# Performance work log

Hardware: AMD Instinct MI355X
Metric: run time of the kernel (lower is better)

## Reference

```python
import jax, jax.numpy as jnp
import numpy as np

N = 50000   # nodes
E = 800000  # edges
D = 128     # input = hidden = output dim
G = 64      # graphs in batch


def setup_inputs() -> dict:
    key = jax.random.key(0)
    ks = jax.random.split(key, 12)
    s = 1.0 / np.sqrt(D)
    x = jax.random.normal(ks[0], (N, D), dtype=jnp.float32)
    edge_index = jax.random.randint(ks[1], (2, E), 0, N, dtype=jnp.int64)
    batch = jnp.sort(jax.random.randint(ks[2], (N,), 0, G, dtype=jnp.int64))
    return {
        "x": x,
        "W1": jax.random.normal(ks[3], (D, D), jnp.float32) * s,
        "b1": jnp.zeros((D,), jnp.float32),
        "W2": jax.random.normal(ks[4], (D, D), jnp.float32) * s,
        "b2": jnp.zeros((D,), jnp.float32),
        "W3": jax.random.normal(ks[5], (D, D), jnp.float32) * s,
        "b3": jnp.zeros((D,), jnp.float32),
        "Wm1": jax.random.normal(ks[6], (D, D), jnp.float32) * s,
        "bm1": jnp.zeros((D,), jnp.float32),
        "Wm2": jax.random.normal(ks[7], (D, D), jnp.float32) * s,
        "bm2": jnp.zeros((D,), jnp.float32),
        "edge_index": edge_index,
        "batch": batch,
    }


def _gcn_conv(x, W, b, src, dst, deg_isqrt, num_nodes):
    # PyG GCNConv: h = D^{-1/2}(A+I)D^{-1/2} X W + b  (self-loops included in src/dst)
    h = x @ W  # [N, Dout]
    norm = deg_isqrt[src] * deg_isqrt[dst]  # [E+N]
    msg = h[src] * norm[:, None]            # gather + scale
    out = jax.ops.segment_sum(msg, dst, num_segments=num_nodes)  # scatter-add
    return out + b


def reference(x, W1, b1, W2, b2, W3, b3, Wm1, bm1, Wm2, bm2, edge_index, batch):
    num_nodes = x.shape[0]
    loop = jnp.arange(num_nodes, dtype=edge_index.dtype)
    src = jnp.concatenate([edge_index[0], loop])  # add self-loops
    dst = jnp.concatenate([edge_index[1], loop])
    # degree with self-loops (edge_weight = 1), computed on target nodes
    deg = jax.ops.segment_sum(jnp.ones_like(dst, dtype=x.dtype), dst,
                              num_segments=num_nodes)
    deg_isqrt = jnp.where(deg > 0, jax.lax.rsqrt(deg), 0.0)

    h = jax.nn.relu(_gcn_conv(x, W1, b1, src, dst, deg_isqrt, num_nodes))
    h = jax.nn.relu(_gcn_conv(h, W2, b2, src, dst, deg_isqrt, num_nodes))
    h = _gcn_conv(h, W3, b3, src, dst, deg_isqrt, num_nodes)

    # global_mean_pool over graph ids
    sums = jax.ops.segment_sum(h, batch, num_segments=G)
    cnts = jax.ops.segment_sum(jnp.ones((num_nodes,), h.dtype), batch,
                               num_segments=G)
    pooled = sums / jnp.maximum(cnts, 1.0)[:, None]  # [G, D]

    out = jax.nn.relu(pooled @ Wm1 + bm1) @ Wm2 + bm2
    return out
```

## Files before the change

kernel.cpp:

```cpp
#include <hip/hip_runtime.h>
#include <hip/hip_bf16.h>

typedef __attribute__((ext_vector_type(8))) short short8;
typedef __attribute__((ext_vector_type(4))) float floatx4;

#define SLAB_CAP 96

static __device__ __forceinline__ ushort f2b(float f) {
    __hip_bfloat16 h = __float2bfloat16(f);
    return __builtin_bit_cast(ushort, h);
}
static __device__ __forceinline__ float blo(uint u) {
    return __builtin_bit_cast(float, u << 16);
}
static __device__ __forceinline__ float bhi(uint u) {
    return __builtin_bit_cast(float, u & 0xffff0000u);
}
static __device__ __forceinline__ uint pack2(float lo, float hi) {
    return (uint)f2b(lo) | ((uint)f2b(hi) << 16);
}

static __device__ __forceinline__ void fill_body(int bid, const int* __restrict__ src,
                                                 const int* __restrict__ dst, int E,
                                                 int* __restrict__ deg_cnt,
                                                 int* __restrict__ slab) {
    int e0 = (bid * 256 + threadIdx.x) * 4;
    if (e0 + 3 < E) {
        int4 s = *(const int4*)(src + e0);
        int4 d = *(const int4*)(dst + e0);
        int p0 = atomicAdd(&deg_cnt[d.x], 1);
        int p1 = atomicAdd(&deg_cnt[d.y], 1);
        int p2 = atomicAdd(&deg_cnt[d.z], 1);
        int p3 = atomicAdd(&deg_cnt[d.w], 1);
        if (p0 < SLAB_CAP) slab[d.x * SLAB_CAP + p0] = s.x;
        if (p1 < SLAB_CAP) slab[d.y * SLAB_CAP + p1] = s.y;
        if (p2 < SLAB_CAP) slab[d.z * SLAB_CAP + p2] = s.z;
        if (p3 < SLAB_CAP) slab[d.w * SLAB_CAP + p3] = s.w;
    } else {
        for (int e = e0; e < E; ++e) {
            int d = dst[e];
            int p = atomicAdd(&deg_cnt[d], 1);
            if (p < SLAB_CAP) slab[d * SLAB_CAP + p] = src[e];
        }
    }
}

template <typename XT, int SCALE>
static __device__ __forceinline__ void mm_body(ushort* __restrict__ wt,
                                               const XT* __restrict__ X,
                                               const float* __restrict__ W,
                                               const int* __restrict__ degp,
                                               ushort* __restrict__ Y,
                                               int N, int tiles, int tile0, int tstride) {
    int t = threadIdx.x;
    {
        int c0 = (t & 31) * 4;
        int k0 = (t >> 5) * 4;
#pragma unroll
        for (int i = 0; i < 4; i++) {
            int kk = k0 + i * 32;
            float4 r0 = *(const float4*)&W[(kk + 0) * 128 + c0];
            float4 r1 = *(const float4*)&W[(kk + 1) * 128 + c0];
            float4 r2 = *(const float4*)&W[(kk + 2) * 128 + c0];
            float4 r3 = *(const float4*)&W[(kk + 3) * 128 + c0];
            float colv[4][4] = {{r0.x, r1.x, r2.x, r3.x},
                                {r0.y, r1.y, r2.y, r3.y},
                                {r0.z, r1.z, r2.z, r3.z},
                                {r0.w, r1.w, r2.w, r3.w}};
#pragma unroll
            for (int j = 0; j < 4; j++) {
                int c = c0 + j;
                int chs = (kk >> 3) ^ (c & 7);
                int idx = c * 128 + (chs << 3) + (kk & 7);
                ushort4 v;
                v.x = f2b(colv[j][0]); v.y = f2b(colv[j][1]);
                v.z = f2b(colv[j][2]); v.w = f2b(colv[j][3]);
                *(ushort4*)&wt[idx] = v;
            }
        }
    }
    __syncthreads();
    int wv = t >> 6;
    int l  = t & 63;
    int lr = l & 15;
    int lk = l >> 4;
    for (int tile = tile0; tile < tiles; tile += tstride) {
        int row = tile * 64 + wv * 16 + lr;
        int rowc = row < N ? row : N - 1;
        short8 a[4];
#pragma unroll
        for (int ks = 0; ks < 4; ks++) {
            int kb = lk * 8 + ks * 32;
            if constexpr (sizeof(XT) == 4) {
                const float* p = (const float*)X + (size_t)rowc * 128 + kb;
                float4 f0 = *(const float4*)p;
                float4 f1 = *(const float4*)(p + 4);
                short8 av;
                av[0] = (short)f2b(f0.x); av[1] = (short)f2b(f0.y);
                av[2] = (short)f2b(f0.z); av[3] = (short)f2b(f0.w);
                av[4] = (short)f2b(f1.x); av[5] = (short)f2b(f1.y);
                av[6] = (short)f2b(f1.z); av[7] = (short)f2b(f1.w);
                a[ks] = av;
            } else {
                a[ks] = *(const short8*)((const ushort*)X + (size_t)rowc * 128 + kb);
            }
        }
        floatx4 acc[8];
#pragma unroll
        for (int ct = 0; ct < 8; ct++) acc[ct] = (floatx4)(0.f);
#pragma unroll
        for (int ct = 0; ct < 8; ct++) {
            int col = ct * 16 + lr;
#pragma unroll
            for (int ks = 0; ks < 4; ks++) {
                int kb = lk * 8 + ks * 32;
                int chs = (kb >> 3) ^ (col & 7);
                short8 b = *(const short8*)&wt[col * 128 + (chs << 3)];
                acc[ct] = __builtin_amdgcn_mfma_f32_16x16x32_bf16(a[ks], b, acc[ct], 0, 0, 0);
            }
        }
        int rbase = tile * 64 + wv * 16 + lk * 4;
        float dr[4] = {1.f, 1.f, 1.f, 1.f};
        if constexpr (SCALE) {
            if (rbase + 3 < N) {
                int4 d4 = *(const int4*)&degp[rbase];
                dr[0] = rsqrtf((float)(d4.x + 1)); dr[1] = rsqrtf((float)(d4.y + 1));
                dr[2] = rsqrtf((float)(d4.z + 1)); dr[3] = rsqrtf((float)(d4.w + 1));
            } else {
#pragma unroll
                for (int r = 0; r < 4; r++)
                    dr[r] = rbase + r < N ? rsqrtf((float)(degp[rbase + r] + 1)) : 0.f;
            }
        }
#pragma unroll
        for (int ct = 0; ct < 8; ct++) {
#pragma unroll
            for (int r = 0; r < 4; r++) {
                int ro = rbase + r;
                if (ro < N) Y[(size_t)ro * 128 + ct * 16 + lr] = f2b(acc[ct][r] * dr[r]);
            }
        }
    }
}

__global__ __launch_bounds__(256) void k_fill_mm(const int* __restrict__ src,
                                                 const int* __restrict__ dst, int E,
                                                 int* __restrict__ deg_cnt,
                                                 int* __restrict__ slab,
                                                 const float* __restrict__ X,
                                                 const float* __restrict__ W,
                                                 ushort* __restrict__ Y,
                                                 int N, int tiles, int fillBlocks) {
    __shared__ ushort wt[128 * 128];
    int bid = blockIdx.x;
    if (bid < fillBlocks) {
        fill_body(bid, src, dst, E, deg_cnt, slab);
        return;
    }
    mm_body<float, 0>(wt, X, W, nullptr, Y, N, tiles, bid - fillBlocks, gridDim.x - fillBlocks);
}

template <typename XT, int SCALE>
__global__ __launch_bounds__(256) void k_matmul_mfma(const XT* __restrict__ X,
                                                     const float* __restrict__ W,
                                                     const int* __restrict__ degp,
                                                     ushort* __restrict__ Y,
                                                     int N, int tiles) {
    __shared__ ushort wt[128 * 128];
    mm_body<XT, SCALE>(wt, X, W, degp, Y, N, tiles, blockIdx.x, gridDim.x);
}

template <int MODE>
__global__ __launch_bounds__(256) void k_aggregate(const uint* __restrict__ H,
                                                   const int* __restrict__ deg_cnt,
                                                   const int* __restrict__ slab,
                                                   const float* __restrict__ bias,
                                                   uint* __restrict__ Y,
                                                   const int* __restrict__ batch,
                                                   float* __restrict__ psums, int N) {
    int t = threadIdx.x;
    int node = blockIdx.x * 4 + (t >> 6);
    int lane = t & 63;
    bool valid = node < N;
    float ax = 0.f, ay = 0.f;
    if (valid) {
        int degn = deg_cnt[node];
        float din = rsqrtf((float)(degn + 1));
        uint hv = H[(size_t)node * 64 + lane];
        if constexpr (MODE == 0) { ax = din * blo(hv); ay = din * bhi(hv); }
        else { ax = blo(hv); ay = bhi(hv); }
        int deg = degn > SLAB_CAP ? SLAB_CAP : degn;
        const int* row = slab + (size_t)node * SLAB_CAP;
        int e = 0;
        if constexpr (MODE == 0) {
            for (; e + 3 < deg; e += 4) {
                int4 i0 = *(const int4*)(row + e);
                int d0 = deg_cnt[i0.x], d1 = deg_cnt[i0.y];
                int d2 = deg_cnt[i0.z], d3 = deg_cnt[i0.w];
                uint g0 = H[(size_t)i0.x * 64 + lane];
                uint g1 = H[(size_t)i0.y * 64 + lane];
                uint g2 = H[(size_t)i0.z * 64 + lane];
                uint g3 = H[(size_t)i0.w * 64 + lane];
                float w0 = rsqrtf((float)(d0 + 1)), w1 = rsqrtf((float)(d1 + 1));
                float w2 = rsqrtf((float)(d2 + 1)), w3 = rsqrtf((float)(d3 + 1));
                ax += blo(g0) * w0 + blo(g1) * w1 + blo(g2) * w2 + blo(g3) * w3;
                ay += bhi(g0) * w0 + bhi(g1) * w1 + bhi(g2) * w2 + bhi(g3) * w3;
            }
            for (; e < deg; ++e) {
                int s = row[e];
                float ws = rsqrtf((float)(deg_cnt[s] + 1));
                uint g = H[(size_t)s * 64 + lane];
                ax += blo(g) * ws; ay += bhi(g) * ws;
            }
        } else {
            float bx = 0.f, by = 0.f;
            for (; e + 7 < deg; e += 8) {
                int4 i0 = *(const int4*)(row + e);
                int4 i1 = *(const int4*)(row + e + 4);
                uint g0 = H[(size_t)i0.x * 64 + lane];
                uint g1 = H[(size_t)i0.y * 64 + lane];
                uint g2 = H[(size_t)i0.z * 64 + lane];
                uint g3 = H[(size_t)i0.w * 64 + lane];
                uint g4 = H[(size_t)i1.x * 64 + lane];
                uint g5 = H[(size_t)i1.y * 64 + lane];
                uint g6 = H[(size_t)i1.z * 64 + lane];
                uint g7 = H[(size_t)i1.w * 64 + lane];
                ax += blo(g0) + blo(g1) + blo(g2) + blo(g3);
                ay += bhi(g0) + bhi(g1) + bhi(g2) + bhi(g3);
                bx += blo(g4) + blo(g5) + blo(g6) + blo(g7);
                by += bhi(g4) + bhi(g5) + bhi(g6) + bhi(g7);
            }
            for (; e + 3 < deg; e += 4) {
                int4 i0 = *(const int4*)(row + e);
                uint g0 = H[(size_t)i0.x * 64 + lane];
                uint g1 = H[(size_t)i0.y * 64 + lane];
                uint g2 = H[(size_t)i0.z * 64 + lane];
                uint g3 = H[(size_t)i0.w * 64 + lane];
                ax += blo(g0) + blo(g1) + blo(g2) + blo(g3);
                ay += bhi(g0) + bhi(g1) + bhi(g2) + bhi(g3);
            }
            for (; e < deg; ++e) {
                uint g = H[(size_t)row[e] * 64 + lane];
                ax += blo(g); ay += bhi(g);
            }
            ax += bx; ay += by;
        }
        float2 b = *(const float2*)&bias[lane * 2];
        ax = ax * din + b.x; ay = ay * din + b.y;
        if constexpr (MODE != 2) {
            ax = fmaxf(ax, 0.f); ay = fmaxf(ay, 0.f);
            Y[(size_t)node * 64 + lane] = pack2(ax, ay);
        }
    }
    if constexpr (MODE == 2) {
        __shared__ float ls[128];
        if (t < 128) ls[t] = 0.f;
        __syncthreads();
        int nbase = blockIdx.x * 4;
        if (nbase >= N) return;
        int nlast = nbase + 3 < N ? nbase + 3 : N - 1;
        int gf = batch[nbase], gl = batch[nlast];
        if (gf == gl) {
            if (valid) {
                atomicAdd(&ls[lane * 2], ax);
                atomicAdd(&ls[lane * 2 + 1], ay);
            }
            __syncthreads();
            if (t < 128) atomicAdd(&psums[gf * 128 + t], ls[t]);
        } else {
            if (valid) {
                int g = batch[node];
                atomicAdd(&psums[g * 128 + lane * 2], ax);
                atomicAdd(&psums[g * 128 + lane * 2 + 1], ay);
            }
        }
    }
}

__global__ __launch_bounds__(128) void k_mlp(const float* __restrict__ sums,
                                             const int* __restrict__ batch, int N,
                                             const float* __restrict__ Wm1,
                                             const float* __restrict__ bm1,
                                             const float* __restrict__ Wm2,
                                             const float* __restrict__ bm2,
                                             float* __restrict__ out) {
    __shared__ float p[128], t1[128];
    int g = blockIdx.x, j = threadIdx.x;
    int n0, n1;
    {
        int lo = 0, hi = N;
        while (lo < hi) { int m = (lo + hi) >> 1; if (batch[m] < g) lo = m + 1; else hi = m; }
        n0 = lo;
        hi = N;
        while (lo < hi) { int m = (lo + hi) >> 1; if (batch[m] < g + 1) lo = m + 1; else hi = m; }
        n1 = lo;
    }
    float cnt = (float)(n1 - n0);
    p[j] = sums[g * 128 + j] / fmaxf(cnt, 1.0f);
    __syncthreads();
    float acc = bm1[j];
#pragma unroll 4
    for (int k = 0; k < 128; k++) acc += p[k] * Wm1[k * 128 + j];
    t1[j] = fmaxf(acc, 0.f);
    __syncthreads();
    float acc2 = bm2[j];
#pragma unroll 4
    for (int k = 0; k < 128; k++) acc2 += t1[k] * Wm2[k * 128 + j];
    out[g * 128 + j] = acc2;
}

extern "C" void kernel_launch(void* const* d_in, const int* in_sizes, int n_in,
                              void* d_out, int out_size, void* d_ws, size_t ws_size,
                              hipStream_t stream) {
    const float* x   = (const float*)d_in[0];
    const float* W1  = (const float*)d_in[1];
    const float* b1  = (const float*)d_in[2];
    const float* W2  = (const float*)d_in[3];
    const float* b2  = (const float*)d_in[4];
    const float* W3  = (const float*)d_in[5];
    const float* b3  = (const float*)d_in[6];
    const float* Wm1 = (const float*)d_in[7];
    const float* bm1 = (const float*)d_in[8];
    const float* Wm2 = (const float*)d_in[9];
    const float* bm2 = (const float*)d_in[10];
    const int* edge  = (const int*)d_in[11];
    const int* batch = (const int*)d_in[12];

    int N = in_sizes[0] / 128;
    int E = in_sizes[11] / 2;
    int G = out_size / 128;
    const int* esrc = edge;
    const int* edst = edge + E;

    char* w = (char*)d_ws;
    auto alloc = [&](size_t bytes) -> char* {
        char* p = w;
        w += (bytes + 255) & ~size_t(255);
        return p;
    };
    ushort* Hb     = (ushort*)alloc((size_t)N * 128 * 2);
    ushort* Gb     = (ushort*)alloc((size_t)N * 128 * 2);
    int*    slab   = (int*)alloc((size_t)N * SLAB_CAP * 4);
    char*  zbase   = w;
    int*   deg_cnt = (int*)alloc((size_t)N * 4);
    float* psums   = (float*)alloc((size_t)G * 128 * 4);
    size_t zbytes  = (size_t)(w - zbase);

    hipMemsetAsync(zbase, 0, zbytes, stream);

    int tiles64 = (N + 63) / 64;
    int fillBlocks = (E + 1023) / 1024;

    k_fill_mm<<<fillBlocks + tiles64, 256, 0, stream>>>(esrc, edst, E, deg_cnt, slab,
                                                        x, W1, Gb, N, tiles64, fillBlocks);
    k_aggregate<0><<<(N + 3) / 4, 256, 0, stream>>>((const uint*)Gb, deg_cnt, slab, b1,
                                                    (uint*)Hb, nullptr, nullptr, N);
    k_matmul_mfma<ushort, 1><<<tiles64, 256, 0, stream>>>(Hb, W2, deg_cnt, Gb, N, tiles64);
    k_aggregate<1><<<(N + 3) / 4, 256, 0, stream>>>((const uint*)Gb, deg_cnt, slab, b2,
                                                    (uint*)Hb, nullptr, nullptr, N);
    k_matmul_mfma<ushort, 1><<<tiles64, 256, 0, stream>>>(Hb, W3, deg_cnt, Gb, N, tiles64);
    k_aggregate<2><<<(N + 3) / 4, 256, 0, stream>>>((const uint*)Gb, deg_cnt, slab, b3,
                                                    nullptr, batch, psums, N);

    k_mlp<<<G, 128, 0, stream>>>(psums, batch, N, Wm1, bm1, Wm2, bm2, (float*)d_out);
}
```

Baseline: 324.9 us.

## Fuse whole GCN pipeline into one persistent cooperative kernel with grid syncs

Replaces the chain of separate launches (memset, fill+matmul, three aggregations, two matmuls, MLP) with a single cooperative persistent kernel that zeroes buffers itself and separates phases with grid.sync(). The first-layer aggregation is restructured: a separate prescale pass multiplies H by the source-node deg^-1/2 so all layers can use the unweighted aggregation path. A non-cooperative multi-kernel fallback is kept. The aim is to remove launch gaps and tail effects; the cost is that grid-wide barriers and a fixed, occupancy-limited grid size (launch bounds 256,4) may lower latency hiding in the gather-heavy aggregations and make the fill/matmul split less balanced.

```diff
diff --git a/kernel.cpp b/kernel.cpp
--- a/kernel.cpp
+++ b/kernel.cpp
@@ -1,5 +1,8 @@
 #include <hip/hip_runtime.h>
 #include <hip/hip_bf16.h>
+#include <hip/hip_cooperative_groups.h>
+
+namespace cg = cooperative_groups;
 
 typedef __attribute__((ext_vector_type(8))) short short8;
 typedef __attribute__((ext_vector_type(4))) float floatx4;
@@ -20,11 +23,11 @@
     return (uint)f2b(lo) | ((uint)f2b(hi) << 16);
 }
 
-static __device__ __forceinline__ void fill_body(int bid, const int* __restrict__ src,
-                                                 const int* __restrict__ dst, int E,
-                                                 int* __restrict__ deg_cnt,
-                                                 int* __restrict__ slab) {
-    int e0 = (bid * 256 + threadIdx.x) * 4;
+static __device__ __forceinline__ void fill_chunk(int c, const int* __restrict__ src,
+                                                  const int* __restrict__ dst, int E,
+                                                  int* __restrict__ deg_cnt,
+                                                  int* __restrict__ slab) {
+    int e0 = c * 1024 + threadIdx.x * 4;
     if (e0 + 3 < E) {
         int4 s = *(const int4*)(src + e0);
         int4 d = *(const int4*)(dst + e0);
@@ -143,77 +146,32 @@
     }
 }
 
-__global__ __launch_bounds__(256) void k_fill_mm(const int* __restrict__ src,
-                                                 const int* __restrict__ dst, int E,
-                                                 int* __restrict__ deg_cnt,
-                                                 int* __restrict__ slab,
-                                                 const float* __restrict__ X,
-                                                 const float* __restrict__ W,
-                                                 ushort* __restrict__ Y,
-                                                 int N, int tiles, int fillBlocks) {
-    __shared__ ushort wt[128 * 128];
-    int bid = blockIdx.x;
-    if (bid < fillBlocks) {
-        fill_body(bid, src, dst, E, deg_cnt, slab);
-        return;
-    }
-    mm_body<float, 0>(wt, X, W, nullptr, Y, N, tiles, bid - fillBlocks, gridDim.x - fillBlocks);
-}
-
-template <typename XT, int SCALE>
-__global__ __launch_bounds__(256) void k_matmul_mfma(const XT* __restrict__ X,
-                                                     const float* __restrict__ W,
-                                                     const int* __restrict__ degp,
-                                                     ushort* __restrict__ Y,
-                                                     int N, int tiles) {
-    __shared__ ushort wt[128 * 128];
-    mm_body<XT, SCALE>(wt, X, W, degp, Y, N, tiles, blockIdx.x, gridDim.x);
-}
-
 template <int MODE>
-__global__ __launch_bounds__(256) void k_aggregate(const uint* __restrict__ H,
-                                                   const int* __restrict__ deg_cnt,
-                                                   const int* __restrict__ slab,
-                                                   const float* __restrict__ bias,
-                                                   uint* __restrict__ Y,
-                                                   const int* __restrict__ batch,
-                                                   float* __restrict__ psums, int N) {
+static __device__ void agg_body(const uint* __restrict__ H,
+                                const int* __restrict__ deg_cnt,
+                                const int* __restrict__ slab,
+                                const float* __restrict__ bias,
+                                uint* __restrict__ Y,
+                                const int* __restrict__ batch,
+                                float* __restrict__ psums,
+                                int N, int bid, int nb) {
+    __shared__ float ls[128];
     int t = threadIdx.x;
-    int node = blockIdx.x * 4 + (t >> 6);
     int lane = t & 63;
-    bool valid = node < N;
-    float ax = 0.f, ay = 0.f;
-    if (valid) {
-        int degn = deg_cnt[node];
-        float din = rsqrtf((float)(degn + 1));
-        uint hv = H[(size_t)node * 64 + lane];
-        if constexpr (MODE == 0) { ax = din * blo(hv); ay = din * bhi(hv); }
-        else { ax = blo(hv); ay = bhi(hv); }
-        int deg = degn > SLAB_CAP ? SLAB_CAP : degn;
-        const int* row = slab + (size_t)node * SLAB_CAP;
-        int e = 0;
-        if constexpr (MODE == 0) {
-            for (; e + 3 < deg; e += 4) {
-                int4 i0 = *(const int4*)(row + e);
-                int d0 = deg_cnt[i0.x], d1 = deg_cnt[i0.y];
-                int d2 = deg_cnt[i0.z], d3 = deg_cnt[i0.w];
-                uint g0 = H[(size_t)i0.x * 64 + lane];
-                uint g1 = H[(size_t)i0.y * 64 + lane];
-                uint g2 = H[(size_t)i0.z * 64 + lane];
-                uint g3 = H[(size_t)i0.w * 64 + lane];
-                float w0 = rsqrtf((float)(d0 + 1)), w1 = rsqrtf((float)(d1 + 1));
-                float w2 = rsqrtf((float)(d2 + 1)), w3 = rsqrtf((float)(d3 + 1));
-                ax += blo(g0) * w0 + blo(g1) * w1 + blo(g2) * w2 + blo(g3) * w3;
-                ay += bhi(g0) * w0 + bhi(g1) * w1 + bhi(g2) * w2 + bhi(g3) * w3;
-            }
-            for (; e < deg; ++e) {
-                int s = row[e];
-                float ws = rsqrtf((float)(deg_cnt[s] + 1));
-                uint g = H[(size_t)s * 64 + lane];
-                ax += blo(g) * ws; ay += bhi(g) * ws;
-            }
-        } else {
+    int groups = (N + 3) >> 2;
+    for (int ga = bid; ga < groups; ga += nb) {
+        int node = ga * 4 + (t >> 6);
+        bool valid = node < N;
+        float ax = 0.f, ay = 0.f;
+        if (valid) {
+            int degn = deg_cnt[node];
+            float din = rsqrtf((float)(degn + 1));
+            uint hv = H[(size_t)node * 64 + lane];
+            ax = blo(hv); ay = bhi(hv);
             float bx = 0.f, by = 0.f;
+            int deg = degn > SLAB_CAP ? SLAB_CAP : degn;
+            const int* row = slab + (size_t)node * SLAB_CAP;
+            int e = 0;
             for (; e + 7 < deg; e += 8) {
                 int4 i0 = *(const int4*)(row + e);
                 int4 i1 = *(const int4*)(row + e + 4);
@@ -244,69 +202,201 @@
                 ax += blo(g); ay += bhi(g);
             }
             ax += bx; ay += by;
-        }
-        float2 b = *(const float2*)&bias[lane * 2];
-        ax = ax * din + b.x; ay = ay * din + b.y;
-        if constexpr (MODE != 2) {
-            ax = fmaxf(ax, 0.f); ay = fmaxf(ay, 0.f);
-            Y[(size_t)node * 64 + lane] = pack2(ax, ay);
-        }
-    }
-    if constexpr (MODE == 2) {
-        __shared__ float ls[128];
-        if (t < 128) ls[t] = 0.f;
+            float2 b = *(const float2*)&bias[lane * 2];
+            ax = ax * din + b.x; ay = ay * din + b.y;
+            if constexpr (MODE == 1) {
+                ax = fmaxf(ax, 0.f); ay = fmaxf(ay, 0.f);
+                Y[(size_t)node * 64 + lane] = pack2(ax, ay);
+            }
+        }
+        if constexpr (MODE == 2) {
+            if (t < 128) ls[t] = 0.f;
+            __syncthreads();
+            int nbase = ga * 4;
+            if (nbase < N) {
+                int nlast = nbase + 3 < N ? nbase + 3 : N - 1;
+                int gf = batch[nbase], gl = batch[nlast];
+                if (gf == gl) {
+                    if (valid) {
+                        atomicAdd(&ls[lane * 2], ax);
+                        atomicAdd(&ls[lane * 2 + 1], ay);
+                    }
+                    __syncthreads();
+                    if (t < 128) atomicAdd(&psums[gf * 128 + t], ls[t]);
+                    __syncthreads();
+                } else {
+                    if (valid) {
+                        int g = batch[node];
+                        atomicAdd(&psums[g * 128 + lane * 2], ax);
+                        atomicAdd(&psums[g * 128 + lane * 2 + 1], ay);
+                    }
+                    __syncthreads();
+                }
+            }
+        }
+    }
+}
+
+static __device__ void mlp_body(const float* __restrict__ sums,
+                                const int* __restrict__ batch, int N, int G,
+                                const float* __restrict__ Wm1, const float* __restrict__ bm1,
+                                const float* __restrict__ Wm2, const float* __restrict__ bm2,
+                                float* __restrict__ out, int bid, int nb) {
+    __shared__ float p[128], t1[128];
+    int t = threadIdx.x;
+    for (int g = bid; g < G; g += nb) {
+        int n0, n1;
+        {
+            int lo = 0, hi = N;
+            while (lo < hi) { int m = (lo + hi) >> 1; if (batch[m] < g) lo = m + 1; else hi = m; }
+            n0 = lo;
+            hi = N;
+            while (lo < hi) { int m = (lo + hi) >> 1; if (batch[m] < g + 1) lo = m + 1; else hi = m; }
+            n1 = lo;
+        }
+        if (t < 128) {
+            float cnt = (float)(n1 - n0);
+            p[t] = sums[g * 128 + t] / fmaxf(cnt, 1.0f);
+        }
         __syncthreads();
-        int nbase = blockIdx.x * 4;
-        if (nbase >= N) return;
-        int nlast = nbase + 3 < N ? nbase + 3 : N - 1;
-        int gf = batch[nbase], gl = batch[nlast];
-        if (gf == gl) {
-            if (valid) {
-                atomicAdd(&ls[lane * 2], ax);
-                atomicAdd(&ls[lane * 2 + 1], ay);
-            }
-            __syncthreads();
-            if (t < 128) atomicAdd(&psums[gf * 128 + t], ls[t]);
+        if (t < 128) {
+            float acc = bm1[t];
+#pragma unroll 4
+            for (int k = 0; k < 128; k++) acc += p[k] * Wm1[k * 128 + t];
+            t1[t] = fmaxf(acc, 0.f);
+        }
+        __syncthreads();
+        if (t < 128) {
+            float acc2 = bm2[t];
+#pragma unroll 4
+            for (int k = 0; k < 128; k++) acc2 += t1[k] * Wm2[k * 128 + t];
+            out[g * 128 + t] = acc2;
+        }
+        __syncthreads();
+    }
+}
+
+__global__ __launch_bounds__(256, 4) void k_gnn(
+    const float* __restrict__ x,
+    const float* __restrict__ W1, const float* __restrict__ b1,
+    const float* __restrict__ W2, const float* __restrict__ b2,
+    const float* __restrict__ W3, const float* __restrict__ b3,
+    const float* __restrict__ Wm1, const float* __restrict__ bm1,
+    const float* __restrict__ Wm2, const float* __restrict__ bm2,
+    const int* __restrict__ esrc, const int* __restrict__ edst,
+    const int* __restrict__ batch,
+    int N, int E, int G,
+    int* __restrict__ deg_cnt, int* __restrict__ slab,
+    ushort* __restrict__ Hb, ushort* __restrict__ Gb,
+    float* __restrict__ psums, float* __restrict__ out) {
+    cg::grid_group grid = cg::this_grid();
+    __shared__ ushort wt[128 * 128];
+    int bid = blockIdx.x, nb = gridDim.x, t = threadIdx.x;
+    int tiles = (N + 63) >> 6;
+
+    {
+        int ztot = N + G * 128;
+        for (int i = bid * 256 + t; i < ztot; i += nb * 256) {
+            if (i < N) deg_cnt[i] = 0; else psums[i - N] = 0.f;
+        }
+    }
+    grid.sync();
+
+    {
+        int F = nb >> 1;
+        int C = (E + 1023) >> 10;
+        if (bid < F) {
+            for (int c = bid; c < C; c += F) fill_chunk(c, esrc, edst, E, deg_cnt, slab);
         } else {
-            if (valid) {
-                int g = batch[node];
-                atomicAdd(&psums[g * 128 + lane * 2], ax);
-                atomicAdd(&psums[g * 128 + lane * 2 + 1], ay);
-            }
-        }
-    }
-}
-
-__global__ __launch_bounds__(128) void k_mlp(const float* __restrict__ sums,
-                                             const int* __restrict__ batch, int N,
-                                             const float* __restrict__ Wm1,
-                                             const float* __restrict__ bm1,
-                                             const float* __restrict__ Wm2,
-                                             const float* __restrict__ bm2,
-                                             float* __restrict__ out) {
-    __shared__ float p[128], t1[128];
-    int g = blockIdx.x, j = threadIdx.x;
-    int n0, n1;
+            mm_body<float, 0>(wt, x, W1, nullptr, Gb, N, tiles, bid - F, nb - F);
+        }
+    }
+    grid.sync();
+
     {
-        int lo = 0, hi = N;
-        while (lo < hi) { int m = (lo + hi) >> 1; if (batch[m] < g) lo = m + 1; else hi = m; }
-        n0 = lo;
-        hi = N;
-        while (lo < hi) { int m = (lo + hi) >> 1; if (batch[m] < g + 1) lo = m + 1; else hi = m; }
-        n1 = lo;
-    }
-    float cnt = (float)(n1 - n0);
-    p[j] = sums[g * 128 + j] / fmaxf(cnt, 1.0f);
-    __syncthreads();
-    float acc = bm1[j];
-#pragma unroll 4
-    for (int k = 0; k < 128; k++) acc += p[k] * Wm1[k * 128 + j];
-    t1[j] = fmaxf(acc, 0.f);
-    __syncthreads();
-    float acc2 = bm2[j];
-#pragma unroll 4
-    for (int k = 0; k < 128; k++) acc2 += t1[k] * Wm2[k * 128 + j];
-    out[g * 128 + j] = acc2;
+        const uint* s = (const uint*)Gb;
+        uint* d = (uint*)Hb;
+        int tot = N * 64;
+        for (int i = bid * 256 + t; i < tot; i += nb * 256) {
+            int n = i >> 6;
+            float din = rsqrtf((float)(deg_cnt[n] + 1));
+            uint u = s[i];
+            d[i] = pack2(blo(u) * din, bhi(u) * din);
+        }
+    }
+    grid.sync();
+
+    agg_body<1>((const uint*)Hb, deg_cnt, slab, b1, (uint*)Gb, nullptr, nullptr, N, bid, nb);
+    grid.sync();
+
+    mm_body<ushort, 1>(wt, Gb, W2, deg_cnt, Hb, N, tiles, bid, nb);
+    grid.sync();
+
+    agg_body<1>((const uint*)Hb, deg_cnt, slab, b2, (uint*)Gb, nullptr, nullptr, N, bid, nb);
+    grid.sync();
+
+    mm_body<ushort, 1>(wt, Gb, W3, deg_cnt, Hb, N, tiles, bid, nb);
+    grid.sync();
+
+    agg_body<2>((const uint*)Hb, deg_cnt, slab, b3, nullptr, batch, psums, N, bid, nb);
+    grid.sync();
+
+    mlp_body(psums, batch, N, G, Wm1, bm1, Wm2, bm2, out, bid, nb);
+}
+
+__global__ __launch_bounds__(256) void k_fillmm_s(const int* __restrict__ src,
+                                                  const int* __restrict__ dst, int E,
+                                                  int* __restrict__ deg_cnt,
+                                                  int* __restrict__ slab,
+                                                  const float* __restrict__ X,
+                                                  const float* __restrict__ W,
+                                                  ushort* __restrict__ Y,
+                                                  int N, int tiles, int fillBlocks) {
+    __shared__ ushort wt[128 * 128];
+    int bid = blockIdx.x;
+    if (bid < fillBlocks) { fill_chunk(bid, src, dst, E, deg_cnt, slab); return; }
+    mm_body<float, 0>(wt, X, W, nullptr, Y, N, tiles, bid - fillBlocks, gridDim.x - fillBlocks);
+}
+
+__global__ __launch_bounds__(256) void k_prescale_s(const int* __restrict__ deg_cnt,
+                                                    const uint* __restrict__ s,
+                                                    uint* __restrict__ d, int N) {
+    int i = blockIdx.x * 256 + threadIdx.x;
+    if (i >= N * 64) return;
+    int n = i >> 6;
+    float din = rsqrtf((float)(deg_cnt[n] + 1));
+    uint u = s[i];
+    d[i] = pack2(blo(u) * din, bhi(u) * din);
+}
+
+template <typename XT, int SCALE>
+__global__ __launch_bounds__(256) void k_mm_s(const XT* __restrict__ X,
+                                              const float* __restrict__ W,
+                                              const int* __restrict__ degp,
+                                              ushort* __restrict__ Y, int N, int tiles) {
+    __shared__ ushort wt[128 * 128];
+    mm_body<XT, SCALE>(wt, X, W, degp, Y, N, tiles, blockIdx.x, gridDim.x);
+}
+
+template <int MODE>
+__global__ __launch_bounds__(256) void k_agg_s(const uint* __restrict__ H,
+                                               const int* __restrict__ deg_cnt,
+                                               const int* __restrict__ slab,
+                                               const float* __restrict__ bias,
+                                               uint* __restrict__ Y,
+                                               const int* __restrict__ batch,
+                                               float* __restrict__ psums, int N) {
+    agg_body<MODE>(H, deg_cnt, slab, bias, Y, batch, psums, N, blockIdx.x, gridDim.x);
+}
+
+__global__ __launch_bounds__(256) void k_mlp_s(const float* __restrict__ sums,
+                                               const int* __restrict__ batch, int N, int G,
+                                               const float* __restrict__ Wm1,
+                                               const float* __restrict__ bm1,
+                                               const float* __restrict__ Wm2,
+                                               const float* __restrict__ bm2,
+                                               float* __restrict__ out) {
+    mlp_body(sums, batch, N, G, Wm1, bm1, Wm2, bm2, out, blockIdx.x, gridDim.x);
 }
 
 extern "C" void kernel_launch(void* const* d_in, const int* in_sizes, int n_in,
@@ -331,6 +421,7 @@
     int G = out_size / 128;
     const int* esrc = edge;
     const int* edst = edge + E;
+    float* out = (float*)d_out;
 
     char* w = (char*)d_ws;
     auto alloc = [&](size_t bytes) -> char* {
@@ -346,21 +437,46 @@
     float* psums   = (float*)alloc((size_t)G * 128 * 4);
     size_t zbytes  = (size_t)(w - zbase);
 
+    int tiles = (N + 63) / 64;
+    int C = (E + 1023) / 1024;
+
+    int perCU = 0, cus = 0, dev = 0;
+    hipGetDevice(&dev);
+    hipDeviceGetAttribute(&cus, hipDeviceAttributeMultiprocessorCount, dev);
+    hipError_t qerr = hipOccupancyMaxActiveBlocksPerMultiprocessor(&perCU, k_gnn, 256, 0);
+    bool coop_ok = (qerr == hipSuccess) && perCU >= 1 && cus >= 1;
+    if (coop_ok) {
+        int nb = perCU * cus;
+        if (nb > 2048) nb = 2048;
+        if (nb < 8) coop_ok = false;
+        if (coop_ok) {
+            const float *a0 = x, *a1 = W1, *a2 = b1, *a3 = W2, *a4 = b2, *a5 = W3, *a6 = b3;
+            const float *a7 = Wm1, *a8 = bm1, *a9 = Wm2, *a10 = bm2;
+            const int *a11 = esrc, *a12 = edst, *a13 = batch;
+            int a14 = N, a15 = E, a16 = G;
+            int *a17 = deg_cnt, *a18 = slab;
+            ushort *a19 = Hb, *a20 = Gb;
+            float *a21 = psums, *a22 = out;
+            void* args[] = {&a0, &a1, &a2, &a3, &a4, &a5, &a6, &a7, &a8, &a9, &a10,
+                            &a11, &a12, &a13, &a14, &a15, &a16, &a17, &a18, &a19,
+                            &a20, &a21, &a22};
+            hipError_t lerr = hipLaunchCooperativeKernel((const void*)k_gnn, dim3(nb),
+                                                         dim3(256), args, 0, stream);
+            if (lerr == hipSuccess) return;
+        }
+    }
+
     hipMemsetAsync(zbase, 0, zbytes, stream);
-
-    int tiles64 = (N + 63) / 64;
-    int fillBlocks = (E + 1023) / 1024;
-
-    k_fill_mm<<<fillBlocks + tiles64, 256, 0, stream>>>(esrc, edst, E, deg_cnt, slab,
-                                                        x, W1, Gb, N, tiles64, fillBlocks);
-    k_aggregate<0><<<(N + 3) / 4, 256, 0, stream>>>((const uint*)Gb, deg_cnt, slab, b1,
-                                                    (uint*)Hb, nullptr, nullptr, N);
-    k_matmul_mfma<ushort, 1><<<tiles64, 256, 0, stream>>>(Hb, W2, deg_cnt, Gb, N, tiles64);
-    k_aggregate<1><<<(N + 3) / 4, 256, 0, stream>>>((const uint*)Gb, deg_cnt, slab, b2,
-                                                    (uint*)Hb, nullptr, nullptr, N);
-    k_matmul_mfma<ushort, 1><<<tiles64, 256, 0, stream>>>(Hb, W3, deg_cnt, Gb, N, tiles64);
-    k_aggregate<2><<<(N + 3) / 4, 256, 0, stream>>>((const uint*)Gb, deg_cnt, slab, b3,
-                                                    nullptr, batch, psums, N);
-
-    k_mlp<<<G, 128, 0, stream>>>(psums, batch, N, Wm1, bm1, Wm2, bm2, (float*)d_out);
-}
+    k_fillmm_s<<<C + tiles, 256, 0, stream>>>(esrc, edst, E, deg_cnt, slab,
+                                              x, W1, Gb, N, tiles, C);
+    k_prescale_s<<<(N * 64 + 255) / 256, 256, 0, stream>>>(deg_cnt, (const uint*)Gb, (uint*)Hb, N);
+    k_agg_s<1><<<(N + 3) / 4, 256, 0, stream>>>((const uint*)Hb, deg_cnt, slab, b1,
+                                                (uint*)Gb, nullptr, nullptr, N);
+    k_mm_s<ushort, 1><<<tiles, 256, 0, stream>>>(Gb, W2, deg_cnt, Hb, N, tiles);
+    k_agg_s<1><<<(N + 3) / 4, 256, 0, stream>>>((const uint*)Hb, deg_cnt, slab, b2,
+                                                (uint*)Gb, nullptr, nullptr, N);
+    k_mm_s<ushort, 1><<<tiles, 256, 0, stream>>>(Gb, W3, deg_cnt, Hb, N, tiles);
+    k_agg_s<2><<<(N + 3) / 4, 256, 0, stream>>>((const uint*)Hb, deg_cnt, slab, b3,
+                                                nullptr, batch, psums, N);
+    k_mlp_s<<<G, 256, 0, stream>>>(psums, batch, N, G, Wm1, bm1, Wm2, bm2, out);
+}
```

Measured after the change: 970.9 us. 2.99x slower.
